# Optimization experiments

Measured on AMD Instinct MI355X. Metric: run time of the kernel, lower is better.

Reference implementation:

```python
import jax, jax.numpy as jnp
import numpy as np

N = 50000      # nodes
E = 1600000    # edges (before self-loops)
IN = 128       # in_chnl
H = 2          # heads
C = 64         # out_chnl per head
NEG_SLOPE = 0.2


def setup_inputs() -> dict:
    key = jax.random.key(0)
    k1, k2, k3, k4, k5 = jax.random.split(key, 5)
    h_node = jax.random.normal(k1, (N, IN), dtype=jnp.float32)
    edge_index = jax.random.randint(k2, (2, E), 0, N, dtype=jnp.int32)
    s = 1.0 / np.sqrt(IN)
    W = (jax.random.normal(k3, (IN, H * C), dtype=jnp.float32) * s)
    att_src = jax.random.normal(k4, (H, C), dtype=jnp.float32) * s
    att_dst = jax.random.normal(k5, (H, C), dtype=jnp.float32) * s
    bias = jnp.zeros((H * C,), dtype=jnp.float32)
    return {"h_node": h_node, "edge_index": edge_index, "W": W,
            "att_src": att_src, "att_dst": att_dst, "bias": bias}


def reference(h_node, edge_index, W, att_src, att_dst, bias):
    # dropout is identity in eval mode
    src, dst = edge_index[0], edge_index[1]
    # PyG GATConv default: add self-loops
    loops = jnp.arange(N, dtype=src.dtype)
    src = jnp.concatenate([src, loops])
    dst = jnp.concatenate([dst, loops])

    x = (h_node @ W).reshape(N, H, C)              # [N,H,C] projected features
    a_s = jnp.sum(x * att_src, axis=-1)            # [N,H] source attention terms
    a_d = jnp.sum(x * att_dst, axis=-1)            # [N,H] dest attention terms

    e = jax.nn.leaky_relu(a_s[src] + a_d[dst], NEG_SLOPE)        # [E+N,H]
    # segment softmax over edges grouped by destination node
    m = jax.lax.stop_gradient(jax.ops.segment_max(e, dst, num_segments=N))
    ex = jnp.exp(e - m[dst])
    den = jax.ops.segment_sum(ex, dst, num_segments=N)           # [N,H]
    alpha = ex / den[dst]                                        # [E+N,H]

    out = jax.ops.segment_sum(alpha[:, :, None] * x[src], dst, num_segments=N)
    out = out.reshape(N, H * C) + bias             # concat=True -> [N, H*C]
    return jax.nn.elu(out)
```

## Files before the change

### kernel.cpp

```cpp
#include <hip/hip_runtime.h>
#include <hip/hip_bf16.h>

#define NN 50000
#define EE 1600000
#define TOT (EE + NN)
#define INC 128
#define HC 128
#define NEG_SLOPE 0.2f

#define EPB 4096
#define NB1 ((TOT + EPB - 1) / EPB)
#define RNG 128
#define NR ((NN + RNG - 1) / RNG)
#define CAPR 4864
#define NPB 4
#define MAXD 136

__device__ __forceinline__ unsigned short f2bf(float f) {
    __hip_bfloat16 b = __float2bfloat16(f);
    return *reinterpret_cast<unsigned short*>(&b);
}

#define LOADW(dst, kk)                                                        \
    _Pragma("unroll") for (int q = 0; q < 4; q++) {                           \
        float4 wv4 = *reinterpret_cast<const float4*>(&W[(size_t)((kk) + q) * HC + j2 * 4]); \
        dst[q][0] = wv4.x; dst[q][1] = wv4.y; dst[q][2] = wv4.z; dst[q][3] = wv4.w; \
    }

#define FMAS(wv, kk)                                                          \
    _Pragma("unroll") for (int r8 = 0; r8 < 8; r8++) {                        \
        float4 hv = *reinterpret_cast<const float4*>(&hs[rg * 8 + r8][kk]);   \
        _Pragma("unroll") for (int c = 0; c < 4; c++)                         \
            acc[r8][c] += hv.x * wv[0][c] + hv.y * wv[1][c]                   \
                        + hv.z * wv[2][c] + hv.w * wv[3][c];                  \
    }

__global__ __launch_bounds__(256) void gat_proj(const float* __restrict__ h,
                                                const float* __restrict__ W,
                                                __hip_bfloat16* __restrict__ x_bf) {
    __shared__ float hs[64][INC];
    const int t = threadIdx.x;
    const int row0 = blockIdx.x * 64;

    for (int q = t; q < 64 * 32; q += 256) {
        int rr = q >> 5;
        int c4 = (q & 31) << 2;
        int gr = row0 + rr;
        float4 v = (gr < NN) ? *reinterpret_cast<const float4*>(&h[(size_t)gr * INC + c4])
                             : make_float4(0.f, 0.f, 0.f, 0.f);
        *reinterpret_cast<float4*>(&hs[rr][c4]) = v;
    }
    __syncthreads();

    const int j2 = t & 31;
    const int rg = t >> 5;
    float acc[8][4];
#pragma unroll
    for (int r8 = 0; r8 < 8; r8++)
#pragma unroll
        for (int c = 0; c < 4; c++) acc[r8][c] = 0.f;

    float wA[4][4], wB[4][4];
    LOADW(wA, 0)
    for (int k = 0; k < INC; k += 8) {
        LOADW(wB, k + 4)
        FMAS(wA, k)
        if (k + 8 < INC) { LOADW(wA, k + 8) }
        FMAS(wB, k + 4)
    }

#pragma unroll
    for (int r8 = 0; r8 < 8; r8++) {
        int gr = row0 + rg * 8 + r8;
        if (gr < NN) {
            ushort4 sv;
            sv.x = f2bf(acc[r8][0]);
            sv.y = f2bf(acc[r8][1]);
            sv.z = f2bf(acc[r8][2]);
            sv.w = f2bf(acc[r8][3]);
            *reinterpret_cast<ushort4*>(&x_bf[(size_t)gr * HC + j2 * 4]) = sv;
        }
    }
}

__global__ __launch_bounds__(256) void gat_att(const unsigned int* __restrict__ x2,
                                               const float2* __restrict__ as2,
                                               const float2* __restrict__ ad2,
                                               float* __restrict__ a_s,
                                               float* __restrict__ a_d) {
    int wv = (blockIdx.x * 256 + threadIdx.x) >> 6;
    int lane = threadIdx.x & 63;
    if (wv >= NN) return;
    unsigned int u = x2[(size_t)wv * 64 + lane];
    float x0 = __uint_as_float(u << 16);
    float x1 = __uint_as_float(u & 0xffff0000u);
    float2 as = as2[lane];
    float2 ad = ad2[lane];
    float ps = x0 * as.x + x1 * as.y;
    float pd = x0 * ad.x + x1 * ad.y;
#pragma unroll
    for (int o = 1; o < 32; o <<= 1) {
        ps += __shfl_xor(ps, o);
        pd += __shfl_xor(pd, o);
    }
    if ((lane & 31) == 0) {
        a_s[wv * 2 + (lane >> 5)] = ps;
        a_d[wv * 2 + (lane >> 5)] = pd;
    }
}

__global__ __launch_bounds__(256) void gat_bin(const int* __restrict__ ei,
                                               unsigned int* __restrict__ gbin,
                                               unsigned short* __restrict__ bofs) {
    __shared__ int cnt[NR];
    __shared__ int ofs[NR + 1];
    __shared__ int cur[NR];
    __shared__ int wsum[4];
    __shared__ unsigned int lbuf[EPB];
    const int t = threadIdx.x;
    const int b = blockIdx.x;

    for (int i = t; i < NR; i += 256) cnt[i] = 0;
    __syncthreads();

    unsigned int pk[16];
    bool vd[16];
#pragma unroll
    for (int q = 0; q < 16; q++) {
        int i = b * EPB + q * 256 + t;
        vd[q] = (i < TOT);
        int s, d;
        if (i < EE)       { s = ei[i]; d = ei[EE + i]; }
        else if (i < TOT) { s = d = i - EE; }
        else              { s = d = 0; }
        pk[q] = ((unsigned int)(d >> 7) << 23) |
                ((unsigned int)(d & 127) << 16) | (unsigned int)s;
        if (vd[q]) atomicAdd(&cnt[pk[q] >> 23], 1);
    }
    __syncthreads();

    {
        int v0 = (2 * t < NR) ? cnt[2 * t] : 0;
        int v1 = (2 * t + 1 < NR) ? cnt[2 * t + 1] : 0;
        int ps = v0 + v1;
        int sc = ps;
        int lane = t & 63, wid = t >> 6;
#pragma unroll
        for (int o = 1; o < 64; o <<= 1) {
            int u = __shfl_up(sc, o);
            if (lane >= o) sc += u;
        }
        if (lane == 63) wsum[wid] = sc;
        __syncthreads();
        int woff = 0;
        for (int ww = 0; ww < wid; ww++) woff += wsum[ww];
        int excl = woff + sc - ps;
        if (2 * t <= NR) ofs[2 * t] = excl;
        if (2 * t < NR) cur[2 * t] = excl;
        if (2 * t + 1 <= NR) ofs[2 * t + 1] = excl + v0;
        if (2 * t + 1 < NR) cur[2 * t + 1] = excl + v0;
    }
    __syncthreads();

#pragma unroll
    for (int q = 0; q < 16; q++) {
        if (vd[q]) {
            int pos = atomicAdd(&cur[pk[q] >> 23], 1);
            lbuf[pos] = pk[q];
        }
    }
    __syncthreads();

#pragma unroll
    for (int q = 0; q < 16; q++)
        gbin[(size_t)b * EPB + q * 256 + t] = lbuf[q * 256 + t];
    for (int i = t; i <= NR; i += 256)
        bofs[(size_t)b * (NR + 1) + i] = (unsigned short)ofs[i];
}

__global__ __launch_bounds__(256) void gat_build(const unsigned int* __restrict__ gbin,
                                                 const unsigned short* __restrict__ bofs,
                                                 unsigned short* __restrict__ csr,
                                                 int* __restrict__ start32,
                                                 int* __restrict__ deg32) {
    __shared__ unsigned int est[CAPR];
    __shared__ int deg[RNG];
    __shared__ int ofs[RNG + 1];
    __shared__ int cur[RNG];
    __shared__ int wsum[4];
    __shared__ int etot;
    const int t = threadIdx.x;
    const int r = blockIdx.x;

    for (int i = t; i < CAPR; i += 256) est[i] = 0xFFFFFFFFu;
    for (int i = t; i < RNG; i += 256) { deg[i] = 0; cur[i] = 0; }
    if (t == 0) etot = 0;
    __syncthreads();

    for (int sb = t; sb < NB1; sb += 256) {
        int o0 = (int)bofs[(size_t)sb * (NR + 1) + r];
        int o1 = (int)bofs[(size_t)sb * (NR + 1) + r + 1];
        int c = o1 - o0;
        if (c <= 0) continue;
        int ao = atomicAdd(&etot, c);
        if (ao + c > CAPR) continue;
        const unsigned int* src = gbin + (size_t)sb * EPB + o0;
        for (int q = 0; q < c; q++) est[ao + q] = src[q];
    }
    __syncthreads();

    const int tot = min(etot, CAPR);
    for (int i = t; i < tot; i += 256) {
        unsigned int e = est[i];
        if (e != 0xFFFFFFFFu) atomicAdd(&deg[(e >> 16) & 127], 1);
    }
    __syncthreads();

    {
        int v = (t < RNG) ? deg[t] : 0;
        int sc = v;
        int lane = t & 63, wid = t >> 6;
#pragma unroll
        for (int o = 1; o < 64; o <<= 1) {
            int u = __shfl_up(sc, o);
            if (lane >= o) sc += u;
        }
        if (lane == 63) wsum[wid] = sc;
        __syncthreads();
        int woff = 0;
        for (int ww = 0; ww < wid; ww++) woff += wsum[ww];
        int excl = woff + sc - v;
        if (t < RNG) ofs[t] = excl;
        if (t == RNG - 1) ofs[RNG] = excl + v;
    }
    __syncthreads();

    const int rbase = r * CAPR;
    for (int i = t; i < tot; i += 256) {
        unsigned int e = est[i];
        if (e == 0xFFFFFFFFu) continue;
        int dl = (e >> 16) & 127;
        int pos = atomicAdd(&cur[dl], 1);
        csr[(size_t)rbase + ofs[dl] + pos] = (unsigned short)(e & 0xFFFFu);
    }
    __syncthreads();

    if (t < RNG) {
        int n = r * RNG + t;
        if (n < NN) {
            start32[n] = rbase + ofs[t];
            deg32[n] = deg[t];
        }
    }
}

__global__ __launch_bounds__(256) void gat_aggr(
        const uint4* __restrict__ x16,
        const float2* __restrict__ a_s2, const float2* __restrict__ a_d2,
        const int* __restrict__ start32, const int* __restrict__ deg32,
        const unsigned short* __restrict__ csr,
        const float4* __restrict__ bias4, float4* __restrict__ out4) {
    __shared__ int    s_src[NPB][MAXD];
    __shared__ float2 s_p[NPB][MAXD];
    const int w    = threadIdx.x >> 6;
    const int lane = threadIdx.x & 63;
    const int n    = blockIdx.x * NPB + w;
    if (n >= NN) return;

    const int deg  = min(deg32[n], MAXD - 4);
    const int base = start32[n];
    const float2 ad = a_d2[n];

    float d0 = 0.f, d1 = 0.f;
    for (int jj = lane; jj < deg; jj += 64) {
        int s = (int)csr[(size_t)base + jj];
        s_src[w][jj] = s;
        float2 as = a_s2[s];
        float e0 = as.x + ad.x; e0 = (e0 > 0.f) ? e0 : NEG_SLOPE * e0;
        float e1 = as.y + ad.y; e1 = (e1 > 0.f) ? e1 : NEG_SLOPE * e1;
        float p0 = __expf(e0), p1 = __expf(e1);
        s_p[w][jj] = make_float2(p0, p1);
        d0 += p0;
        d1 += p1;
    }
    if (lane < 4) {
        s_src[w][deg + lane] = 0;
        s_p[w][deg + lane] = make_float2(0.f, 0.f);
    }
#pragma unroll
    for (int off = 32; off; off >>= 1) {
        d0 += __shfl_xor(d0, off);
        d1 += __shfl_xor(d1, off);
    }

    const int sub = lane >> 4;
    const int cl  = lane & 15;
    const int hd  = cl >> 3;
    const float* __restrict__ pwl = &s_p[w][0].x + hd;

    float a0=0.f,a1=0.f,a2=0.f,a3=0.f,a4=0.f,a5=0.f,a6=0.f,a7=0.f;
    const int ng = (deg + 3) >> 2;
    int g = 0;
    for (; g + 4 <= ng; g += 4) {
#pragma unroll
        for (int k = 0; k < 4; k++) {
            int e = 4 * (g + k) + sub;
            int s = s_src[w][e];
            uint4 u = x16[(size_t)s * 16 + cl];
            float wk = pwl[2 * e];
            a0 += wk * __uint_as_float(u.x << 16);
            a1 += wk * __uint_as_float(u.x & 0xffff0000u);
            a2 += wk * __uint_as_float(u.y << 16);
            a3 += wk * __uint_as_float(u.y & 0xffff0000u);
            a4 += wk * __uint_as_float(u.z << 16);
            a5 += wk * __uint_as_float(u.z & 0xffff0000u);
            a6 += wk * __uint_as_float(u.w << 16);
            a7 += wk * __uint_as_float(u.w & 0xffff0000u);
        }
    }
    for (; g < ng; g++) {
        int e = 4 * g + sub;
        int s = s_src[w][e];
        uint4 u = x16[(size_t)s * 16 + cl];
        float wk = pwl[2 * e];
        a0 += wk * __uint_as_float(u.x << 16);
        a1 += wk * __uint_as_float(u.x & 0xffff0000u);
        a2 += wk * __uint_as_float(u.y << 16);
        a3 += wk * __uint_as_float(u.y & 0xffff0000u);
        a4 += wk * __uint_as_float(u.z << 16);
        a5 += wk * __uint_as_float(u.z & 0xffff0000u);
        a6 += wk * __uint_as_float(u.w << 16);
        a7 += wk * __uint_as_float(u.w & 0xffff0000u);
    }
#define MRG(a) a += __shfl_xor(a, 16); a += __shfl_xor(a, 32);
    MRG(a0) MRG(a1) MRG(a2) MRG(a3) MRG(a4) MRG(a5) MRG(a6) MRG(a7)
#undef MRG

    if (lane < 16) {
        const float invd = 1.0f / (hd ? d1 : d0);
        float4 b0 = bias4[cl * 2];
        float4 b1 = bias4[cl * 2 + 1];
        float4 o0, o1;
        o0.x = a0 * invd + b0.x;  o0.y = a1 * invd + b0.y;
        o0.z = a2 * invd + b0.z;  o0.w = a3 * invd + b0.w;
        o1.x = a4 * invd + b1.x;  o1.y = a5 * invd + b1.y;
        o1.z = a6 * invd + b1.z;  o1.w = a7 * invd + b1.w;
        o0.x = (o0.x > 0.f) ? o0.x : expm1f(o0.x);
        o0.y = (o0.y > 0.f) ? o0.y : expm1f(o0.y);
        o0.z = (o0.z > 0.f) ? o0.z : expm1f(o0.z);
        o0.w = (o0.w > 0.f) ? o0.w : expm1f(o0.w);
        o1.x = (o1.x > 0.f) ? o1.x : expm1f(o1.x);
        o1.y = (o1.y > 0.f) ? o1.y : expm1f(o1.y);
        o1.z = (o1.z > 0.f) ? o1.z : expm1f(o1.z);
        o1.w = (o1.w > 0.f) ? o1.w : expm1f(o1.w);
        out4[(size_t)n * 32 + cl * 2] = o0;
        out4[(size_t)n * 32 + cl * 2 + 1] = o1;
    }
}

static inline size_t align256(size_t v) { return (v + 255) & ~(size_t)255; }

extern "C" void kernel_launch(void* const* d_in, const int* in_sizes, int n_in,
                              void* d_out, int out_size, void* d_ws, size_t ws_size,
                              hipStream_t stream) {
    const float* h_node  = (const float*)d_in[0];
    const int*   ei      = (const int*)d_in[1];
    const float* W       = (const float*)d_in[2];
    const float* att_src = (const float*)d_in[3];
    const float* att_dst = (const float*)d_in[4];
    const float* bias    = (const float*)d_in[5];
    float* out = (float*)d_out;

    char* base = (char*)d_ws;
    size_t off = 0;
    __hip_bfloat16* x_bf = (__hip_bfloat16*)(base + off);
    off = align256(off + (size_t)NN * HC * 2);
    float* a_s = (float*)(base + off);      off = align256(off + (size_t)NN * 2 * 4);
    float* a_d = (float*)(base + off);      off = align256(off + (size_t)NN * 2 * 4);
    unsigned int* gbin = (unsigned int*)(base + off);
    off = align256(off + (size_t)NB1 * EPB * 4);
    unsigned short* bofs = (unsigned short*)(base + off);
    off = align256(off + (size_t)NB1 * (NR + 1) * 2);
    unsigned short* csr = (unsigned short*)(base + off);
    off = align256(off + (size_t)NR * CAPR * 2);
    int* start32 = (int*)(base + off);      off = align256(off + (size_t)NN * 4);
    int* deg32 = (int*)(base + off);        off = align256(off + (size_t)NN * 4);
    (void)ws_size;

    gat_proj<<<(NN + 63) / 64, 256, 0, stream>>>(h_node, W, x_bf);
    gat_att<<<(NN + 3) / 4, 256, 0, stream>>>((const unsigned int*)x_bf,
                                              (const float2*)att_src,
                                              (const float2*)att_dst, a_s, a_d);
    gat_bin<<<NB1, 256, 0, stream>>>(ei, gbin, bofs);
    gat_build<<<NR, 256, 0, stream>>>(gbin, bofs, csr, start32, deg32);
    gat_aggr<<<(NN + NPB - 1) / NPB, 256, 0, stream>>>((const uint4*)x_bf,
                                                       (const float2*)a_s,
                                                       (const float2*)a_d,
                                                       start32, deg32, csr,
                                                       (const float4*)bias,
                                                       (float4*)out);
}
```

Measured before the change: 216.1 us.

## Fuse attention logits into projection and rework edge binning and CSR build

```diff
diff --git a/kernel.cpp b/kernel.cpp
--- a/kernel.cpp
+++ b/kernel.cpp
@@ -8,9 +8,11 @@
 #define HC 128
 #define NEG_SLOPE 0.2f
 
-#define EPB 4096
+#define EPB 8192
 #define NB1 ((TOT + EPB - 1) / EPB)
 #define RNG 128
+#define NR ((NN + RNG - 1) / NR_DUMMY)
+#undef NR
 #define NR ((NN + RNG - 1) / RNG)
 #define CAPR 4864
 #define NPB 4
@@ -37,7 +39,11 @@
 
 __global__ __launch_bounds__(256) void gat_proj(const float* __restrict__ h,
                                                 const float* __restrict__ W,
-                                                __hip_bfloat16* __restrict__ x_bf) {
+                                                const float* __restrict__ att_src,
+                                                const float* __restrict__ att_dst,
+                                                __hip_bfloat16* __restrict__ x_bf,
+                                                float* __restrict__ a_s,
+                                                float* __restrict__ a_d) {
     __shared__ float hs[64][INC];
     const int t = threadIdx.x;
     const int row0 = blockIdx.x * 64;
@@ -81,31 +87,27 @@
             *reinterpret_cast<ushort4*>(&x_bf[(size_t)gr * HC + j2 * 4]) = sv;
         }
     }
-}
-
-__global__ __launch_bounds__(256) void gat_att(const unsigned int* __restrict__ x2,
-                                               const float2* __restrict__ as2,
-                                               const float2* __restrict__ ad2,
-                                               float* __restrict__ a_s,
-                                               float* __restrict__ a_d) {
-    int wv = (blockIdx.x * 256 + threadIdx.x) >> 6;
-    int lane = threadIdx.x & 63;
-    if (wv >= NN) return;
-    unsigned int u = x2[(size_t)wv * 64 + lane];
-    float x0 = __uint_as_float(u << 16);
-    float x1 = __uint_as_float(u & 0xffff0000u);
-    float2 as = as2[lane];
-    float2 ad = ad2[lane];
-    float ps = x0 * as.x + x1 * as.y;
-    float pd = x0 * ad.x + x1 * ad.y;
-#pragma unroll
-    for (int o = 1; o < 32; o <<= 1) {
-        ps += __shfl_xor(ps, o);
-        pd += __shfl_xor(pd, o);
-    }
-    if ((lane & 31) == 0) {
-        a_s[wv * 2 + (lane >> 5)] = ps;
-        a_d[wv * 2 + (lane >> 5)] = pd;
+
+    const int lane = t & 63;
+    const int hidx = j2 >> 4;
+    const float4 avs = *reinterpret_cast<const float4*>(&att_src[j2 * 4]);
+    const float4 avd = *reinterpret_cast<const float4*>(&att_dst[j2 * 4]);
+#pragma unroll
+    for (int r8 = 0; r8 < 8; r8++) {
+        float ps = acc[r8][0] * avs.x + acc[r8][1] * avs.y
+                 + acc[r8][2] * avs.z + acc[r8][3] * avs.w;
+        float pd = acc[r8][0] * avd.x + acc[r8][1] * avd.y
+                 + acc[r8][2] * avd.z + acc[r8][3] * avd.w;
+#pragma unroll
+        for (int o = 1; o < 16; o <<= 1) {
+            ps += __shfl_xor(ps, o);
+            pd += __shfl_xor(pd, o);
+        }
+        int gr = row0 + rg * 8 + r8;
+        if ((lane & 15) == 0 && gr < NN) {
+            a_s[gr * 2 + hidx] = ps;
+            a_d[gr * 2 + hidx] = pd;
+        }
     }
 }
 
@@ -116,26 +118,18 @@
     __shared__ int ofs[NR + 1];
     __shared__ int cur[NR];
     __shared__ int wsum[4];
-    __shared__ unsigned int lbuf[EPB];
     const int t = threadIdx.x;
     const int b = blockIdx.x;
 
     for (int i = t; i < NR; i += 256) cnt[i] = 0;
     __syncthreads();
 
-    unsigned int pk[16];
-    bool vd[16];
-#pragma unroll
-    for (int q = 0; q < 16; q++) {
+#pragma unroll 4
+    for (int q = 0; q < 32; q++) {
         int i = b * EPB + q * 256 + t;
-        vd[q] = (i < TOT);
-        int s, d;
-        if (i < EE)       { s = ei[i]; d = ei[EE + i]; }
-        else if (i < TOT) { s = d = i - EE; }
-        else              { s = d = 0; }
-        pk[q] = ((unsigned int)(d >> 7) << 23) |
-                ((unsigned int)(d & 127) << 16) | (unsigned int)s;
-        if (vd[q]) atomicAdd(&cnt[pk[q] >> 23], 1);
+        if (i >= TOT) continue;
+        int d = (i < EE) ? ei[EE + i] : (i - EE);
+        atomicAdd(&cnt[d >> 7], 1);
     }
     __syncthreads();
 
@@ -162,18 +156,18 @@
     }
     __syncthreads();
 
-#pragma unroll
-    for (int q = 0; q < 16; q++) {
-        if (vd[q]) {
-            int pos = atomicAdd(&cur[pk[q] >> 23], 1);
-            lbuf[pos] = pk[q];
-        }
-    }
-    __syncthreads();
-
-#pragma unroll
-    for (int q = 0; q < 16; q++)
-        gbin[(size_t)b * EPB + q * 256 + t] = lbuf[q * 256 + t];
+#pragma unroll 4
+    for (int q = 0; q < 32; q++) {
+        int i = b * EPB + q * 256 + t;
+        if (i >= TOT) continue;
+        int s, d;
+        if (i < EE) { s = ei[i]; d = ei[EE + i]; }
+        else        { s = d = i - EE; }
+        int pos = atomicAdd(&cur[d >> 7], 1);
+        gbin[(size_t)b * EPB + pos] = ((unsigned int)(d & 127) << 16) | (unsigned int)s;
+    }
+    __syncthreads();
+
     for (int i = t; i <= NR; i += 256)
         bofs[(size_t)b * (NR + 1) + i] = (unsigned short)ofs[i];
 }
@@ -191,35 +185,52 @@
     __shared__ int etot;
     const int t = threadIdx.x;
     const int r = blockIdx.x;
-
-    for (int i = t; i < CAPR; i += 256) est[i] = 0xFFFFFFFFu;
+    const int lane = t & 63, wid = t >> 6;
+
     for (int i = t; i < RNG; i += 256) { deg[i] = 0; cur[i] = 0; }
     if (t == 0) etot = 0;
     __syncthreads();
 
-    for (int sb = t; sb < NB1; sb += 256) {
-        int o0 = (int)bofs[(size_t)sb * (NR + 1) + r];
-        int o1 = (int)bofs[(size_t)sb * (NR + 1) + r + 1];
-        int c = o1 - o0;
-        if (c <= 0) continue;
-        int ao = atomicAdd(&etot, c);
-        if (ao + c > CAPR) continue;
-        const unsigned int* src = gbin + (size_t)sb * EPB + o0;
-        for (int q = 0; q < c; q++) est[ao + q] = src[q];
+    {
+        const int cb = wid * 64;
+        int sb = cb + lane;
+        int c = 0, o0 = 0;
+        if (sb < NB1) {
+            o0 = (int)bofs[(size_t)sb * (NR + 1) + r];
+            int o1 = (int)bofs[(size_t)sb * (NR + 1) + r + 1];
+            c = o1 - o0;
+        }
+        int sc = c;
+#pragma unroll
+        for (int o = 1; o < 64; o <<= 1) {
+            int u = __shfl_up(sc, o);
+            if (lane >= o) sc += u;
+        }
+        int wtot = __shfl(sc, 63);
+        int bse = 0;
+        if (lane == 63 && wtot > 0) bse = atomicAdd(&etot, wtot);
+        bse = __shfl(bse, 63);
+        int loc = bse + sc - c;
+        for (int j = 0; j < 64; j++) {
+            int cj = __shfl(c, j);
+            if (cj <= 0) continue;
+            int oj = __shfl(o0, j);
+            int lj = __shfl(loc, j);
+            const unsigned int* src = gbin + (size_t)(cb + j) * EPB + oj;
+            for (int q = lane; q < cj; q += 64)
+                if (lj + q < CAPR) est[lj + q] = src[q];
+        }
     }
     __syncthreads();
 
     const int tot = min(etot, CAPR);
-    for (int i = t; i < tot; i += 256) {
-        unsigned int e = est[i];
-        if (e != 0xFFFFFFFFu) atomicAdd(&deg[(e >> 16) & 127], 1);
-    }
+    for (int i = t; i < tot; i += 256)
+        atomicAdd(&deg[(est[i] >> 16) & 127], 1);
     __syncthreads();
 
     {
         int v = (t < RNG) ? deg[t] : 0;
         int sc = v;
-        int lane = t & 63, wid = t >> 6;
 #pragma unroll
         for (int o = 1; o < 64; o <<= 1) {
             int u = __shfl_up(sc, o);
@@ -238,7 +249,6 @@
     const int rbase = r * CAPR;
     for (int i = t; i < tot; i += 256) {
         unsigned int e = est[i];
-        if (e == 0xFFFFFFFFu) continue;
         int dl = (e >> 16) & 127;
         int pos = atomicAdd(&cur[dl], 1);
         csr[(size_t)rbase + ofs[dl] + pos] = (unsigned short)(e & 0xFFFFu);
@@ -387,10 +397,8 @@
     int* deg32 = (int*)(base + off);        off = align256(off + (size_t)NN * 4);
     (void)ws_size;
 
-    gat_proj<<<(NN + 63) / 64, 256, 0, stream>>>(h_node, W, x_bf);
-    gat_att<<<(NN + 3) / 4, 256, 0, stream>>>((const unsigned int*)x_bf,
-                                              (const float2*)att_src,
-                                              (const float2*)att_dst, a_s, a_d);
+    gat_proj<<<(NN + 63) / 64, 256, 0, stream>>>(h_node, W, att_src, att_dst,
+                                                 x_bf, a_s, a_d);
     gat_bin<<<NB1, 256, 0, stream>>>(ei, gbin, bofs);
     gat_build<<<NR, 256, 0, stream>>>(gbin, bofs, csr, start32, deg32);
     gat_aggr<<<(NN + NPB - 1) / NPB, 256, 0, stream>>>((const uint4*)x_bf,
```

Measured after the change: 240.8 us. 11.4% more time.

## Fuse projection, attention scores and edge binning into one launch

Applied to the files above, without the earlier changes.

```diff
diff --git a/kernel.cpp b/kernel.cpp
--- a/kernel.cpp
+++ b/kernel.cpp
@@ -15,6 +15,7 @@
 #define CAPR 4864
 #define NPB 4
 #define MAXD 136
+#define PROJB ((NN + 63) / 64)
 
 __device__ __forceinline__ unsigned short f2bf(float f) {
     __hip_bfloat16 b = __float2bfloat16(f);
@@ -29,18 +30,22 @@
 
 #define FMAS(wv, kk)                                                          \
     _Pragma("unroll") for (int r8 = 0; r8 < 8; r8++) {                        \
-        float4 hv = *reinterpret_cast<const float4*>(&hs[rg * 8 + r8][kk]);   \
+        const float* hr = hs + (rg * 8 + r8) * INC + (kk);                    \
+        float4 hv = *reinterpret_cast<const float4*>(hr);                     \
         _Pragma("unroll") for (int c = 0; c < 4; c++)                         \
             acc[r8][c] += hv.x * wv[0][c] + hv.y * wv[1][c]                   \
                         + hv.z * wv[2][c] + hv.w * wv[3][c];                  \
     }
 
-__global__ __launch_bounds__(256) void gat_proj(const float* __restrict__ h,
-                                                const float* __restrict__ W,
-                                                __hip_bfloat16* __restrict__ x_bf) {
-    __shared__ float hs[64][INC];
+__device__ __forceinline__ void proj_body(
+        char* smem, int pb,
+        const float* __restrict__ h, const float* __restrict__ W,
+        const float* __restrict__ att_src, const float* __restrict__ att_dst,
+        __hip_bfloat16* __restrict__ x_bf,
+        float* __restrict__ a_s, float* __restrict__ a_d) {
+    float* hs = (float*)smem;
     const int t = threadIdx.x;
-    const int row0 = blockIdx.x * 64;
+    const int row0 = pb * 64;
 
     for (int q = t; q < 64 * 32; q += 256) {
         int rr = q >> 5;
@@ -48,7 +53,7 @@
         int gr = row0 + rr;
         float4 v = (gr < NN) ? *reinterpret_cast<const float4*>(&h[(size_t)gr * INC + c4])
                              : make_float4(0.f, 0.f, 0.f, 0.f);
-        *reinterpret_cast<float4*>(&hs[rr][c4]) = v;
+        *reinterpret_cast<float4*>(&hs[rr * INC + c4]) = v;
     }
     __syncthreads();
 
@@ -81,44 +86,40 @@
             *reinterpret_cast<ushort4*>(&x_bf[(size_t)gr * HC + j2 * 4]) = sv;
         }
     }
-}
-
-__global__ __launch_bounds__(256) void gat_att(const unsigned int* __restrict__ x2,
-                                               const float2* __restrict__ as2,
-                                               const float2* __restrict__ ad2,
-                                               float* __restrict__ a_s,
-                                               float* __restrict__ a_d) {
-    int wv = (blockIdx.x * 256 + threadIdx.x) >> 6;
-    int lane = threadIdx.x & 63;
-    if (wv >= NN) return;
-    unsigned int u = x2[(size_t)wv * 64 + lane];
-    float x0 = __uint_as_float(u << 16);
-    float x1 = __uint_as_float(u & 0xffff0000u);
-    float2 as = as2[lane];
-    float2 ad = ad2[lane];
-    float ps = x0 * as.x + x1 * as.y;
-    float pd = x0 * ad.x + x1 * ad.y;
-#pragma unroll
-    for (int o = 1; o < 32; o <<= 1) {
-        ps += __shfl_xor(ps, o);
-        pd += __shfl_xor(pd, o);
-    }
-    if ((lane & 31) == 0) {
-        a_s[wv * 2 + (lane >> 5)] = ps;
-        a_d[wv * 2 + (lane >> 5)] = pd;
-    }
-}
-
-__global__ __launch_bounds__(256) void gat_bin(const int* __restrict__ ei,
-                                               unsigned int* __restrict__ gbin,
-                                               unsigned short* __restrict__ bofs) {
-    __shared__ int cnt[NR];
-    __shared__ int ofs[NR + 1];
-    __shared__ int cur[NR];
-    __shared__ int wsum[4];
-    __shared__ unsigned int lbuf[EPB];
+
+    const int lane = t & 63;
+    const int hidx = j2 >> 4;
+    const float4 avs = *reinterpret_cast<const float4*>(&att_src[j2 * 4]);
+    const float4 avd = *reinterpret_cast<const float4*>(&att_dst[j2 * 4]);
+#pragma unroll
+    for (int r8 = 0; r8 < 8; r8++) {
+        float ps = acc[r8][0] * avs.x + acc[r8][1] * avs.y
+                 + acc[r8][2] * avs.z + acc[r8][3] * avs.w;
+        float pd = acc[r8][0] * avd.x + acc[r8][1] * avd.y
+                 + acc[r8][2] * avd.z + acc[r8][3] * avd.w;
+#pragma unroll
+        for (int o = 1; o < 16; o <<= 1) {
+            ps += __shfl_xor(ps, o);
+            pd += __shfl_xor(pd, o);
+        }
+        int gr = row0 + rg * 8 + r8;
+        if ((lane & 15) == 0 && gr < NN) {
+            a_s[gr * 2 + hidx] = ps;
+            a_d[gr * 2 + hidx] = pd;
+        }
+    }
+}
+
+__device__ __forceinline__ void bin_body(
+        char* smem, int b,
+        const int* __restrict__ ei,
+        unsigned int* __restrict__ gbin, unsigned short* __restrict__ bofs) {
+    int* cnt = (int*)smem;
+    int* ofs = cnt + NR;
+    int* cur = ofs + NR + 1;
+    int* wsum = cur + NR;
+    unsigned int* lbuf = (unsigned int*)(wsum + 4);
     const int t = threadIdx.x;
-    const int b = blockIdx.x;
 
     for (int i = t; i < NR; i += 256) cnt[i] = 0;
     __syncthreads();
@@ -176,6 +177,20 @@
         gbin[(size_t)b * EPB + q * 256 + t] = lbuf[q * 256 + t];
     for (int i = t; i <= NR; i += 256)
         bofs[(size_t)b * (NR + 1) + i] = (unsigned short)ofs[i];
+}
+
+__global__ __launch_bounds__(256) void gat_fused1(
+        const float* __restrict__ h, const float* __restrict__ W,
+        const float* __restrict__ att_src, const float* __restrict__ att_dst,
+        const int* __restrict__ ei,
+        unsigned int* __restrict__ gbin, unsigned short* __restrict__ bofs,
+        __hip_bfloat16* __restrict__ x_bf,
+        float* __restrict__ a_s, float* __restrict__ a_d) {
+    __shared__ __align__(16) char smem[64 * INC * 4];
+    if (blockIdx.x < NB1)
+        bin_body(smem, blockIdx.x, ei, gbin, bofs);
+    else
+        proj_body(smem, blockIdx.x - NB1, h, W, att_src, att_dst, x_bf, a_s, a_d);
 }
 
 __global__ __launch_bounds__(256) void gat_build(const unsigned int* __restrict__ gbin,
@@ -387,11 +402,8 @@
     int* deg32 = (int*)(base + off);        off = align256(off + (size_t)NN * 4);
     (void)ws_size;
 
-    gat_proj<<<(NN + 63) / 64, 256, 0, stream>>>(h_node, W, x_bf);
-    gat_att<<<(NN + 3) / 4, 256, 0, stream>>>((const unsigned int*)x_bf,
-                                              (const float2*)att_src,
-                                              (const float2*)att_dst, a_s, a_d);
-    gat_bin<<<NB1, 256, 0, stream>>>(ei, gbin, bofs);
+    gat_fused1<<<NB1 + PROJB, 256, 0, stream>>>(h_node, W, att_src, att_dst, ei,
+                                                gbin, bofs, x_bf, a_s, a_d);
     gat_build<<<NR, 256, 0, stream>>>(gbin, bofs, csr, start32, deg32);
     gat_aggr<<<(NN + NPB - 1) / NPB, 256, 0, stream>>>((const uint4*)x_bf,
                                                        (const float2*)a_s,
```

Measured after the change: 202.6 us. 6.3% less time.
